# Optimization experiments

Measured on AMD Instinct MI355X. Metric: run time of the kernel, lower is better.

Reference implementation:

```python
import jax, jax.numpy as jnp
import numpy as np

B, L, ENC, EMB, H, V = 64, 33, 512, 256, 512, 32000


def setup_inputs() -> dict:
    key = jax.random.key(0)
    ks = jax.random.split(key, 16)
    x = jax.random.normal(ks[0], (B, ENC), dtype=jnp.float32)
    padded_target = jax.random.randint(ks[1], (B, L), 0, V)
    target_lengths = jax.random.randint(ks[2], (B,), 2, L + 1)
    target_lengths = target_lengths.at[0].set(L)  # pin max length -> static step count
    s = 0.05
    return {
        "x": x,
        "padded_target": padded_target,
        "target_lengths": target_lengths,
        "embed": jax.random.normal(ks[3], (V, EMB), dtype=jnp.float32) * s,
        "W_h0": jax.random.normal(ks[4], (H, ENC), dtype=jnp.float32) * s,
        "b_h0": jnp.zeros((H,), jnp.float32),
        "W_c0": jax.random.normal(ks[5], (H, ENC), dtype=jnp.float32) * s,
        "b_c0": jnp.zeros((H,), jnp.float32),
        "W_ih": jax.random.normal(ks[6], (4 * H, ENC + EMB), dtype=jnp.float32) * s,
        "W_hh": jax.random.normal(ks[7], (4 * H, H), dtype=jnp.float32) * s,
        "b_ih": jnp.zeros((4 * H,), jnp.float32),
        "b_hh": jnp.zeros((4 * H,), jnp.float32),
        "W_out": jax.random.normal(ks[8], (V, H), dtype=jnp.float32) * s,
        "b_out": jnp.zeros((V,), jnp.float32),
    }


def reference(x, padded_target, target_lengths, embed, W_h0, b_h0, W_c0, b_c0,
              W_ih, W_hh, b_ih, b_hh, W_out, b_out):
    # sort by length, descending (packed-sequence ordering)
    sorted_indices = jnp.argsort(-target_lengths)
    x = x[sorted_indices]                      # [B, ENC]
    tgt = padded_target[sorted_indices]        # [B, L]
    lens = target_lengths[sorted_indices] - 1  # decode steps per row
    emb = embed[tgt]                           # [B, L, EMB]

    h = x @ W_h0.T + b_h0                      # context-initialized state
    c = x @ W_c0.T + b_c0
    T = padded_target.shape[1] - 1             # static max steps (max len pinned to L)

    def step(carry, inp):
        h, c = carry
        e_t, t = inp
        active = (lens > t)[:, None]           # rows still decoding (prefix, sorted)
        g = jnp.concatenate([x, e_t], axis=1) @ W_ih.T + b_ih + h @ W_hh.T + b_hh
        i, f, gg, o = jnp.split(g, 4, axis=1)  # torch LSTMCell gate order i,f,g,o
        c_new = jax.nn.sigmoid(f) * c + jax.nn.sigmoid(i) * jnp.tanh(gg)
        h_new = jax.nn.sigmoid(o) * jnp.tanh(c_new)
        h = jnp.where(active, h_new, h)        # inactive rows keep frozen state
        c = jnp.where(active, c_new, c)
        pred = jnp.where(active, h_new @ W_out.T + b_out, 0.0)  # dropout p=0
        return (h, c), pred

    (_, _), preds = jax.lax.scan(
        step, (h, c), (jnp.transpose(emb[:, :T], (1, 0, 2)), jnp.arange(T)))
    prediction = jnp.transpose(preds, (1, 0, 2))  # [B, T, V]
    return prediction, sorted_indices
```

## Files before the change

kernel.cpp:

```cpp
#include <hip/hip_runtime.h>

typedef __attribute__((ext_vector_type(8))) short short8;
typedef __attribute__((ext_vector_type(8))) unsigned short ushort8;
typedef __attribute__((ext_vector_type(4))) float f32x4;
typedef __attribute__((ext_vector_type(4))) unsigned short ushort4v;

#define DEV __device__ __forceinline__

DEV unsigned short f2bf(float f) {
  unsigned int u = __float_as_uint(f);
  u += 0x7fffu + ((u >> 16) & 1u);
  return (unsigned short)(u >> 16);
}
DEV float sigm(float x) { return 1.f / (1.f + __expf(-x)); }
DEV float tanh_(float x) { return 1.f - 2.f / (1.f + __expf(2.f * x)); }

typedef __attribute__((address_space(1))) const void* as1cv;
typedef __attribute__((address_space(3))) void* as3v;
DEV void gll16(const void* g, void* l) {
  __builtin_amdgcn_global_load_lds((as1cv)g, (as3v)l, 16, 0, 0);
}

__global__ void __launch_bounds__(256) k_sort(const float* __restrict__ x,
    const int* __restrict__ ptar, const int* __restrict__ tlen,
    int* __restrict__ sidx, int* __restrict__ lens, int* __restrict__ tok,
    float* __restrict__ xs, float* __restrict__ tail) {
  __shared__ int ss[64];
  int tid = threadIdx.x;
  if (tid < 64) {
    int li = tlen[tid];
    int rank = 0;
    for (int j = 0; j < 64; ++j) {
      int lj = tlen[j];
      rank += (lj > li || (lj == li && j < tid)) ? 1 : 0;
    }
    ss[rank] = tid;
  }
  __syncthreads();
  if (tid < 64) {
    int src = ss[tid];
    sidx[tid] = src;
    lens[tid] = tlen[src] - 1;
    tail[tid] = (float)src;
  }
  __syncthreads();
  for (int idx = tid; idx < 32 * 64; idx += 256) {
    int t = idx >> 6, b = idx & 63;
    tok[idx] = ptar[ss[b] * 33 + t];
  }
  for (int idx = tid; idx < 64 * 512; idx += 256) {
    int b = idx >> 9;
    xs[idx] = x[ss[b] * 512 + (idx & 511)];
  }
}

__global__ void __launch_bounds__(256) k_convmany(
    const float* __restrict__ W_h0, const float* __restrict__ W_c0,
    const float* __restrict__ W_ih, const float* __restrict__ W_hh,
    const float* __restrict__ xs,
    unsigned short* __restrict__ Wpro, unsigned short* __restrict__ Wihb2,
    unsigned short* __restrict__ Whb, unsigned short* __restrict__ xsb) {
  long long g = (long long)(blockIdx.x * 256 + threadIdx.x) * 8;
  const float* src;
  unsigned short* dst;
  if (g < 262144) {
    src = W_h0 + g; dst = Wpro + g;
  } else if (g < 524288) {
    long long l = g - 262144; src = W_c0 + l; dst = Wpro + 262144 + l;
  } else if (g < 1572864) {
    long long l = g - 524288;
    long long r = l >> 9, c = l & 511;
    src = W_ih + r * 768 + c; dst = Wpro + 524288 + l;
  } else if (g < 2097152) {
    long long l = g - 1572864;
    long long r = l >> 8, c = l & 255;
    src = W_ih + r * 768 + 512 + c; dst = Wihb2 + l;
  } else if (g < 3145728) {
    long long l = g - 2097152; src = W_hh + l; dst = Whb + l;
  } else {
    long long l = g - 3145728; src = xs + l; dst = xsb + l;
  }
  float4 v0 = *(const float4*)src, v1 = *(const float4*)(src + 4);
  ushort8 o;
  o[0] = f2bf(v0.x); o[1] = f2bf(v0.y); o[2] = f2bf(v0.z); o[3] = f2bf(v0.w);
  o[4] = f2bf(v1.x); o[5] = f2bf(v1.y); o[6] = f2bf(v1.z); o[7] = f2bf(v1.w);
  *(ushort8*)dst = o;
}

__global__ void __launch_bounds__(256) k_conv(const float* __restrict__ W,
    unsigned short* __restrict__ Wb) {
  size_t i = (size_t)(blockIdx.x * 256 + threadIdx.x) * 4;
  float4 v = *(const float4*)(W + i);
  ushort4v o;
  o.x = f2bf(v.x); o.y = f2bf(v.y); o.z = f2bf(v.z); o.w = f2bf(v.w);
  *(ushort4v*)(Wb + i) = o;
}

__global__ void __launch_bounds__(256) k_pro(const unsigned short* __restrict__ xsb,
    const unsigned short* __restrict__ Wpro, const float* __restrict__ b_h0,
    const float* __restrict__ b_c0, const float* __restrict__ b_ih,
    const float* __restrict__ b_hh, unsigned short* __restrict__ h0b,
    float* __restrict__ c, float* __restrict__ gx) {
  int tid = threadIdx.x, lane = tid & 63, w = tid >> 6;
  int n0 = blockIdx.x * 64 + w * 16;
  int lr = lane & 15, lk = lane >> 4;
  f32x4 acc[4];
#pragma unroll
  for (int i = 0; i < 4; ++i) acc[i] = (f32x4){0.f, 0.f, 0.f, 0.f};
  const unsigned short* B = Wpro + (size_t)(n0 + lr) * 512 + lk * 8;
  const unsigned short* A = xsb + (size_t)lr * 512 + lk * 8;
#pragma unroll
  for (int ks = 0; ks < 16; ++ks) {
    short8 bfr = *(const short8*)(B + ks * 32);
#pragma unroll
    for (int mi = 0; mi < 4; ++mi) {
      short8 af = *(const short8*)(A + mi * 16 * 512 + ks * 32);
      acc[mi] = __builtin_amdgcn_mfma_f32_16x16x32_bf16(af, bfr, acc[mi], 0, 0, 0);
    }
  }
  int n = n0 + lr;
#pragma unroll
  for (int mi = 0; mi < 4; ++mi)
#pragma unroll
    for (int r = 0; r < 4; ++r) {
      int b = mi * 16 + lk * 4 + r;
      float v = acc[mi][r];
      if (n < 512) {
        h0b[b * 512 + n] = f2bf(v + b_h0[n]);
      } else if (n < 1024) {
        int u = n - 512;
        c[b * 512 + u] = v + b_c0[u];
      } else {
        int j = n - 1024;
        gx[(size_t)b * 2048 + j] = v + b_ih[j] + b_hh[j];
      }
    }
}

__global__ void __launch_bounds__(256) k_emb(const int* __restrict__ tok,
    const float* __restrict__ embed, unsigned short* __restrict__ Eb) {
  int gid = blockIdx.x * 256 + threadIdx.x;
  int row = gid >> 5, c8 = (gid & 31) * 8;
  const float* src = embed + (size_t)tok[row] * 256 + c8;
  float4 v0 = *(const float4*)src, v1 = *(const float4*)(src + 4);
  ushort8 o;
  o[0] = f2bf(v0.x); o[1] = f2bf(v0.y); o[2] = f2bf(v0.z); o[3] = f2bf(v0.w);
  o[4] = f2bf(v1.x); o[5] = f2bf(v1.y); o[6] = f2bf(v1.z); o[7] = f2bf(v1.w);
  *(ushort8*)(Eb + (size_t)row * 256 + c8) = o;
}

__global__ void __launch_bounds__(256) k_ga2(const unsigned short* __restrict__ Eb,
    const unsigned short* __restrict__ Wb2, const float* __restrict__ gx,
    float* __restrict__ GA) {
  __shared__ alignas(16) char ldsbuf[32768];
  char* ldsA = ldsbuf;
  char* ldsB = ldsbuf + 16384;
  int bid = blockIdx.x;
  int mt = bid & 15, nt = bid >> 4;
  int m0 = mt * 128, n0 = nt * 128;
  int tid = threadIdx.x, lane = tid & 63, w = tid >> 6;
  int wm = w >> 1, wn = w & 1;
  f32x4 acc[4][4];
#pragma unroll
  for (int a = 0; a < 4; ++a)
#pragma unroll
    for (int bq = 0; bq < 4; ++bq) acc[a][bq] = (f32x4){0.f, 0.f, 0.f, 0.f};
  const unsigned short* Arow = Eb + (size_t)m0 * 256;
  const unsigned short* Brow = Wb2 + (size_t)n0 * 256;
  for (int kt = 0; kt < 4; ++kt) {
    int k0 = kt * 64;
    if (kt) __syncthreads();
#pragma unroll
    for (int j = 0; j < 4; ++j) {
      int ci = j * 256 + w * 64 + lane;
      int r = ci >> 3;
      int clog = ((ci & 7) << 4) ^ ((r & 7) << 4);
      int ldst = (j * 256 + w * 64) * 16;
      gll16((const char*)(Arow + (size_t)r * 256 + k0) + clog, ldsA + ldst);
      gll16((const char*)(Brow + (size_t)r * 256 + k0) + clog, ldsB + ldst);
    }
    __syncthreads();
#pragma unroll
    for (int kk = 0; kk < 2; ++kk) {
      short8 af[4], bf[4];
      int cb = kk * 64 + (lane >> 4) * 16;
#pragma unroll
      for (int i = 0; i < 4; ++i) {
        int ar = wm * 64 + i * 16 + (lane & 15);
        af[i] = *(const short8*)(ldsA + ar * 128 + (cb ^ ((ar & 7) << 4)));
        int br = wn * 64 + i * 16 + (lane & 15);
        bf[i] = *(const short8*)(ldsB + br * 128 + (cb ^ ((br & 7) << 4)));
      }
#pragma unroll
      for (int mi = 0; mi < 4; ++mi)
#pragma unroll
        for (int ni = 0; ni < 4; ++ni)
          acc[mi][ni] = __builtin_amdgcn_mfma_f32_16x16x32_bf16(
              af[mi], bf[ni], acc[mi][ni], 0, 0, 0);
    }
  }
#pragma unroll
  for (int mi = 0; mi < 4; ++mi) {
    int mb = m0 + wm * 64 + mi * 16 + ((lane >> 4) << 2);
#pragma unroll
    for (int r = 0; r < 4; ++r) {
      int m = mb + r;
#pragma unroll
      for (int ni = 0; ni < 4; ++ni) {
        int j = n0 + wn * 64 + ni * 16 + (lane & 15);
        GA[(size_t)m * 2048 + j] = acc[mi][ni][r] + gx[(size_t)(m & 63) * 2048 + j];
      }
    }
  }
}

__global__ void __launch_bounds__(256) k_step2(
    const unsigned short* __restrict__ hin, unsigned short* __restrict__ hout,
    float* __restrict__ c, const float* __restrict__ GA,
    const unsigned short* __restrict__ Whb, const int* __restrict__ lens,
    unsigned short* __restrict__ Hm, int t) {
  __shared__ float Gs[4][32][16];
  int tid = threadIdx.x, lane = tid & 63, g = tid >> 6;
  int bk = blockIdx.x, mh = bk & 1, u0 = (bk >> 1) * 16;
  int lr = lane & 15, lk = lane >> 4;
  f32x4 acc[2];
  acc[0] = (f32x4){0.f, 0.f, 0.f, 0.f};
  acc[1] = (f32x4){0.f, 0.f, 0.f, 0.f};
  const unsigned short* B = Whb + (size_t)(g * 512 + u0 + lr) * 512 + lk * 8;
  const unsigned short* A = hin + (size_t)(mh * 32 + lr) * 512 + lk * 8;
#pragma unroll
  for (int ks = 0; ks < 16; ++ks) {
    short8 bfr = *(const short8*)(B + ks * 32);
    short8 a0 = *(const short8*)(A + ks * 32);
    short8 a1 = *(const short8*)(A + 16 * 512 + ks * 32);
    acc[0] = __builtin_amdgcn_mfma_f32_16x16x32_bf16(a0, bfr, acc[0], 0, 0, 0);
    acc[1] = __builtin_amdgcn_mfma_f32_16x16x32_bf16(a1, bfr, acc[1], 0, 0, 0);
  }
  const float* gab = GA + (size_t)(t * 64 + mh * 32) * 2048 + g * 512 + u0 + lr;
#pragma unroll
  for (int mi = 0; mi < 2; ++mi)
#pragma unroll
    for (int r = 0; r < 4; ++r) {
      int rl = mi * 16 + lk * 4 + r;
      Gs[g][rl][lr] = acc[mi][r] + gab[(size_t)rl * 2048];
    }
  __syncthreads();
#pragma unroll
  for (int cell = tid; cell < 512; cell += 256) {
    int row = cell >> 4, uc = cell & 15;
    int b = mh * 32 + row, u = u0 + uc;
    float fi = Gs[0][row][uc], ff = Gs[1][row][uc];
    float fg = Gs[2][row][uc], fo = Gs[3][row][uc];
    float cold = c[b * 512 + u];
    float cn = sigm(ff) * cold + sigm(fi) * tanh_(fg);
    float hn = sigm(fo) * tanh_(cn);
    bool act = lens[b] > t;
    if (act) c[b * 512 + u] = cn;
    unsigned short hb = f2bf(hn);
    hout[b * 512 + u] = act ? hb : hin[b * 512 + u];
    Hm[((size_t)b * 32 + t) * 512 + u] = act ? hb : (unsigned short)0;
  }
}

__global__ void __launch_bounds__(256) k_gemm(const unsigned short* __restrict__ Hm,
    const unsigned short* __restrict__ Wb, const float* __restrict__ b_out,
    const int* __restrict__ lens, float* __restrict__ out) {
  __shared__ alignas(16) char ldsbuf[32768];
  char* ldsA = ldsbuf;
  char* ldsB = ldsbuf + 16384;
  int bid = blockIdx.x;
  int mt = bid & 15, nt = bid >> 4;
  int m0 = mt * 128, n0 = nt * 128;
  int tid = threadIdx.x, lane = tid & 63, w = tid >> 6;
  int wm = w >> 1, wn = w & 1;
  f32x4 acc[4][4];
#pragma unroll
  for (int a = 0; a < 4; ++a)
#pragma unroll
    for (int bq = 0; bq < 4; ++bq) acc[a][bq] = (f32x4){0.f, 0.f, 0.f, 0.f};
  const unsigned short* Arow = Hm + (size_t)m0 * 512;
  const unsigned short* Brow = Wb + (size_t)n0 * 512;
  for (int kt = 0; kt < 8; ++kt) {
    int k0 = kt * 64;
    if (kt) __syncthreads();
#pragma unroll
    for (int j = 0; j < 4; ++j) {
      int ci = j * 256 + w * 64 + lane;
      int r = ci >> 3;
      int clog = ((ci & 7) << 4) ^ ((r & 7) << 4);
      int ldst = (j * 256 + w * 64) * 16;
      gll16((const char*)(Arow + (size_t)r * 512 + k0) + clog, ldsA + ldst);
      gll16((const char*)(Brow + (size_t)r * 512 + k0) + clog, ldsB + ldst);
    }
    __syncthreads();
#pragma unroll
    for (int kk = 0; kk < 2; ++kk) {
      short8 af[4], bf[4];
      int cb = kk * 64 + (lane >> 4) * 16;
#pragma unroll
      for (int i = 0; i < 4; ++i) {
        int ar = wm * 64 + i * 16 + (lane & 15);
        af[i] = *(const short8*)(ldsA + ar * 128 + (cb ^ ((ar & 7) << 4)));
        int br = wn * 64 + i * 16 + (lane & 15);
        bf[i] = *(const short8*)(ldsB + br * 128 + (cb ^ ((br & 7) << 4)));
      }
#pragma unroll
      for (int mi = 0; mi < 4; ++mi)
#pragma unroll
        for (int ni = 0; ni < 4; ++ni)
          acc[mi][ni] = __builtin_amdgcn_mfma_f32_16x16x32_bf16(
              af[mi], bf[ni], acc[mi][ni], 0, 0, 0);
    }
  }
#pragma unroll
  for (int mi = 0; mi < 4; ++mi) {
    int mb = m0 + wm * 64 + mi * 16 + ((lane >> 4) << 2);
#pragma unroll
    for (int r = 0; r < 4; ++r) {
      int m = mb + r;
      int b = m >> 5, t = m & 31;
      bool act = lens[b] > t;
      size_t orow = (size_t)m * 32000;
#pragma unroll
      for (int ni = 0; ni < 4; ++ni) {
        int n = n0 + wn * 64 + ni * 16 + (lane & 15);
        out[orow + n] = act ? (acc[mi][ni][r] + b_out[n]) : 0.f;
      }
    }
  }
}

extern "C" void kernel_launch(void* const* d_in, const int* in_sizes, int n_in,
                              void* d_out, int out_size, void* d_ws, size_t ws_size,
                              hipStream_t stream) {
  const float* x     = (const float*)d_in[0];
  const int*   ptar  = (const int*)d_in[1];
  const int*   tlen  = (const int*)d_in[2];
  const float* embed = (const float*)d_in[3];
  const float* W_h0  = (const float*)d_in[4];
  const float* b_h0  = (const float*)d_in[5];
  const float* W_c0  = (const float*)d_in[6];
  const float* b_c0  = (const float*)d_in[7];
  const float* W_ih  = (const float*)d_in[8];
  const float* W_hh  = (const float*)d_in[9];
  const float* b_ih  = (const float*)d_in[10];
  const float* b_hh  = (const float*)d_in[11];
  const float* W_out = (const float*)d_in[12];
  const float* b_out = (const float*)d_in[13];
  float* out = (float*)d_out;

  char* ws = (char*)d_ws;
  size_t off = 0;
  auto alloc = [&](size_t bytes) {
    void* p = ws + off;
    off += (bytes + 255) & ~(size_t)255;
    return p;
  };
  unsigned short* Wob = (unsigned short*)alloc(32000ull * 512 * 2);
  unsigned short* Hm  = (unsigned short*)alloc(2048ull * 512 * 2);
  float* xs   = (float*)alloc(64 * 512 * 4);
  unsigned short* h0b = (unsigned short*)alloc(64 * 512 * 2);
  unsigned short* h1b = (unsigned short*)alloc(64 * 512 * 2);
  float* cbuf = (float*)alloc(64 * 512 * 4);
  float* gx   = (float*)alloc(64 * 2048 * 4);
  int* sidx = (int*)alloc(64 * 4);
  int* lens = (int*)alloc(64 * 4);
  int* tok  = (int*)alloc(2048 * 4);

  float* GA = out;
  unsigned short* Wpro  = (unsigned short*)(out + 4194304);
  unsigned short* Wihb2 = (unsigned short*)(out + 4980736);
  unsigned short* Whb   = (unsigned short*)(out + 5242880);
  unsigned short* Eb    = (unsigned short*)(out + 5767168);
  unsigned short* xsb   = (unsigned short*)(out + 6029312);
  float* tail = out + 65536000;

  k_sort<<<1, 256, 0, stream>>>(x, ptar, tlen, sidx, lens, tok, xs, tail);
  k_convmany<<<1552, 256, 0, stream>>>(W_h0, W_c0, W_ih, W_hh, xs,
                                       Wpro, Wihb2, Whb, xsb);
  k_conv<<<16000, 256, 0, stream>>>(W_out, Wob);
  k_pro<<<48, 256, 0, stream>>>(xsb, Wpro, b_h0, b_c0, b_ih, b_hh, h0b, cbuf, gx);
  k_emb<<<256, 256, 0, stream>>>(tok, embed, Eb);
  k_ga2<<<256, 256, 0, stream>>>(Eb, Wihb2, gx, GA);

  unsigned short* hb[2] = {h0b, h1b};
  for (int t = 0; t < 32; ++t)
    k_step2<<<64, 256, 0, stream>>>(hb[t & 1], hb[(t + 1) & 1], cbuf, GA, Whb,
                                    lens, Hm, t);

  k_gemm<<<4000, 256, 0, stream>>>(Hm, Wob, b_out, lens, out);
  (void)in_sizes; (void)n_in; (void)out_size; (void)ws_size;
}
```

Before: 448.9 us.

## Compact active rows for output GEMM, fuse W_out conversion, retile step and GEMM

Builds a packed list of active (batch, step) rows so the vocabulary projection GEMM computes only the rows that are still decoding and scatters them back through an inverse index. Inactive output rows are zeroed by a separate fill kernel. The W_out bf16 conversion is merged into the gate-precompute kernel as extra blocks, and the recurrent step kernel is split into more blocks with smaller tiles. The GEMM moves to 512-thread blocks with 128x256 tiles and a grouped block order. This skips wasted GEMM work at the cost of scattered row writes and extra launches and indexing.

Result: faster. 362.4 us (-19.3%).

```diff
diff --git a/kernel.cpp b/kernel.cpp
--- a/kernel.cpp
+++ b/kernel.cpp
@@ -3,7 +3,6 @@
 typedef __attribute__((ext_vector_type(8))) short short8;
 typedef __attribute__((ext_vector_type(8))) unsigned short ushort8;
 typedef __attribute__((ext_vector_type(4))) float f32x4;
-typedef __attribute__((ext_vector_type(4))) unsigned short ushort4v;
 
 #define DEV __device__ __forceinline__
 
@@ -23,9 +22,10 @@
 
 __global__ void __launch_bounds__(256) k_sort(const float* __restrict__ x,
     const int* __restrict__ ptar, const int* __restrict__ tlen,
-    int* __restrict__ sidx, int* __restrict__ lens, int* __restrict__ tok,
+    int* __restrict__ sidx, int* __restrict__ lens, int* __restrict__ base,
+    int* __restrict__ inv, int* __restrict__ Pw, int* __restrict__ tok,
     float* __restrict__ xs, float* __restrict__ tail) {
-  __shared__ int ss[64];
+  __shared__ int ss[64], ls[64], bs[64];
   int tid = threadIdx.x;
   if (tid < 64) {
     int li = tlen[tid];
@@ -40,10 +40,22 @@
   if (tid < 64) {
     int src = ss[tid];
     sidx[tid] = src;
-    lens[tid] = tlen[src] - 1;
+    int l = tlen[src] - 1;
+    ls[tid] = l;
+    lens[tid] = l;
     tail[tid] = (float)src;
   }
   __syncthreads();
+  if (tid == 0) {
+    int s = 0;
+    for (int b = 0; b < 64; ++b) { bs[b] = s; base[b] = s; s += ls[b]; }
+    Pw[0] = s;
+  }
+  __syncthreads();
+  for (int idx = tid; idx < 2048; idx += 256) {
+    int b = idx >> 5, t = idx & 31;
+    if (t < ls[b]) inv[bs[b] + t] = idx;
+  }
   for (int idx = tid; idx < 32 * 64; idx += 256) {
     int t = idx >> 6, b = idx & 63;
     tok[idx] = ptar[ss[b] * 33 + t];
@@ -87,15 +99,6 @@
   *(ushort8*)dst = o;
 }
 
-__global__ void __launch_bounds__(256) k_conv(const float* __restrict__ W,
-    unsigned short* __restrict__ Wb) {
-  size_t i = (size_t)(blockIdx.x * 256 + threadIdx.x) * 4;
-  float4 v = *(const float4*)(W + i);
-  ushort4v o;
-  o.x = f2bf(v.x); o.y = f2bf(v.y); o.z = f2bf(v.z); o.w = f2bf(v.w);
-  *(ushort4v*)(Wb + i) = o;
-}
-
 __global__ void __launch_bounds__(256) k_pro(const unsigned short* __restrict__ xsb,
     const unsigned short* __restrict__ Wpro, const float* __restrict__ b_h0,
     const float* __restrict__ b_c0, const float* __restrict__ b_ih,
@@ -151,14 +154,30 @@
 
 __global__ void __launch_bounds__(256) k_ga2(const unsigned short* __restrict__ Eb,
     const unsigned short* __restrict__ Wb2, const float* __restrict__ gx,
-    float* __restrict__ GA) {
+    float* __restrict__ GA, const float* __restrict__ W_out,
+    unsigned short* __restrict__ Wob) {
+  int bid = blockIdx.x;
+  int tid = threadIdx.x;
+  if (bid >= 256) {
+    long long basei = (long long)(bid - 256) * 65536;
+#pragma unroll 4
+    for (int it = 0; it < 32; ++it) {
+      long long i = basei + (long long)it * 2048 + tid * 8;
+      float4 v0 = *(const float4*)(W_out + i);
+      float4 v1 = *(const float4*)(W_out + i + 4);
+      ushort8 o;
+      o[0] = f2bf(v0.x); o[1] = f2bf(v0.y); o[2] = f2bf(v0.z); o[3] = f2bf(v0.w);
+      o[4] = f2bf(v1.x); o[5] = f2bf(v1.y); o[6] = f2bf(v1.z); o[7] = f2bf(v1.w);
+      *(ushort8*)(Wob + i) = o;
+    }
+    return;
+  }
   __shared__ alignas(16) char ldsbuf[32768];
   char* ldsA = ldsbuf;
   char* ldsB = ldsbuf + 16384;
-  int bid = blockIdx.x;
   int mt = bid & 15, nt = bid >> 4;
   int m0 = mt * 128, n0 = nt * 128;
-  int tid = threadIdx.x, lane = tid & 63, w = tid >> 6;
+  int lane = tid & 63, w = tid >> 6;
   int wm = w >> 1, wn = w & 1;
   f32x4 acc[4][4];
 #pragma unroll
@@ -214,65 +233,74 @@
   }
 }
 
-__global__ void __launch_bounds__(256) k_step2(
+__global__ void __launch_bounds__(256) k_step3(
     const unsigned short* __restrict__ hin, unsigned short* __restrict__ hout,
     float* __restrict__ c, const float* __restrict__ GA,
     const unsigned short* __restrict__ Whb, const int* __restrict__ lens,
-    unsigned short* __restrict__ Hm, int t) {
-  __shared__ float Gs[4][32][16];
+    const int* __restrict__ base, unsigned short* __restrict__ Hm, int t) {
+  __shared__ float Gs[4][16][16];
   int tid = threadIdx.x, lane = tid & 63, g = tid >> 6;
-  int bk = blockIdx.x, mh = bk & 1, u0 = (bk >> 1) * 16;
   int lr = lane & 15, lk = lane >> 4;
-  f32x4 acc[2];
-  acc[0] = (f32x4){0.f, 0.f, 0.f, 0.f};
-  acc[1] = (f32x4){0.f, 0.f, 0.f, 0.f};
-  const unsigned short* B = Whb + (size_t)(g * 512 + u0 + lr) * 512 + lk * 8;
-  const unsigned short* A = hin + (size_t)(mh * 32 + lr) * 512 + lk * 8;
+  int mq = blockIdx.x & 3, ug = blockIdx.x >> 2;
+  int r0 = mq * 16, u0 = ug * 16;
+
+  const float* gab = GA + ((size_t)t * 64 + r0) * 2048 + g * 512 + u0 + lr;
+  float gv[4];
+#pragma unroll
+  for (int r = 0; r < 4; ++r) gv[r] = gab[(size_t)(lk * 4 + r) * 2048];
+
+  const unsigned short* Bp = Whb + (size_t)(g * 512 + u0 + lr) * 512 + lk * 8;
+  const unsigned short* Ap = hin + (size_t)(r0 + lr) * 512 + lk * 8;
+  f32x4 acc = (f32x4){0.f, 0.f, 0.f, 0.f};
 #pragma unroll
   for (int ks = 0; ks < 16; ++ks) {
-    short8 bfr = *(const short8*)(B + ks * 32);
-    short8 a0 = *(const short8*)(A + ks * 32);
-    short8 a1 = *(const short8*)(A + 16 * 512 + ks * 32);
-    acc[0] = __builtin_amdgcn_mfma_f32_16x16x32_bf16(a0, bfr, acc[0], 0, 0, 0);
-    acc[1] = __builtin_amdgcn_mfma_f32_16x16x32_bf16(a1, bfr, acc[1], 0, 0, 0);
-  }
-  const float* gab = GA + (size_t)(t * 64 + mh * 32) * 2048 + g * 512 + u0 + lr;
-#pragma unroll
-  for (int mi = 0; mi < 2; ++mi)
-#pragma unroll
-    for (int r = 0; r < 4; ++r) {
-      int rl = mi * 16 + lk * 4 + r;
-      Gs[g][rl][lr] = acc[mi][r] + gab[(size_t)rl * 2048];
-    }
+    short8 a0 = *(const short8*)(Ap + ks * 32);
+    short8 b0 = *(const short8*)(Bp + ks * 32);
+    acc = __builtin_amdgcn_mfma_f32_16x16x32_bf16(a0, b0, acc, 0, 0, 0);
+  }
+#pragma unroll
+  for (int r = 0; r < 4; ++r) Gs[g][lk * 4 + r][lr] = acc[r] + gv[r];
   __syncthreads();
-#pragma unroll
-  for (int cell = tid; cell < 512; cell += 256) {
-    int row = cell >> 4, uc = cell & 15;
-    int b = mh * 32 + row, u = u0 + uc;
-    float fi = Gs[0][row][uc], ff = Gs[1][row][uc];
-    float fg = Gs[2][row][uc], fo = Gs[3][row][uc];
-    float cold = c[b * 512 + u];
-    float cn = sigm(ff) * cold + sigm(fi) * tanh_(fg);
-    float hn = sigm(fo) * tanh_(cn);
-    bool act = lens[b] > t;
-    if (act) c[b * 512 + u] = cn;
-    unsigned short hb = f2bf(hn);
-    hout[b * 512 + u] = act ? hb : hin[b * 512 + u];
-    Hm[((size_t)b * 32 + t) * 512 + u] = act ? hb : (unsigned short)0;
-  }
-}
-
-__global__ void __launch_bounds__(256) k_gemm(const unsigned short* __restrict__ Hm,
+
+  int row = tid >> 4, uc = tid & 15;
+  int b = r0 + row, u = u0 + uc;
+  float fi = Gs[0][row][uc], ff = Gs[1][row][uc];
+  float fg = Gs[2][row][uc], fo = Gs[3][row][uc];
+  float cold = c[b * 512 + u];
+  float cn = sigm(ff) * cold + sigm(fi) * tanh_(fg);
+  float hn = sigm(fo) * tanh_(cn);
+  bool act = lens[b] > t;
+  if (act) c[b * 512 + u] = cn;
+  unsigned short hbv = f2bf(hn);
+  hout[b * 512 + u] = act ? hbv : hin[b * 512 + u];
+  if (act) Hm[((size_t)(base[b] + t)) * 512 + u] = hbv;
+}
+
+__global__ void __launch_bounds__(256) k_zf(const int* __restrict__ lens,
+    float* __restrict__ out) {
+  int m = blockIdx.x;
+  int b = m >> 5, t = m & 31;
+  if (lens[b] > t) return;
+  float4 z = {0.f, 0.f, 0.f, 0.f};
+  float* row = out + (size_t)m * 32000;
+  for (int i = threadIdx.x * 4; i < 32000; i += 1024)
+    *(float4*)(row + i) = z;
+}
+
+__global__ void __launch_bounds__(512) k_gemm(const unsigned short* __restrict__ Hm,
     const unsigned short* __restrict__ Wb, const float* __restrict__ b_out,
-    const int* __restrict__ lens, float* __restrict__ out) {
-  __shared__ alignas(16) char ldsbuf[32768];
+    const int* __restrict__ inv, const int* __restrict__ Pw,
+    float* __restrict__ out) {
+  __shared__ alignas(16) char ldsbuf[49152];
   char* ldsA = ldsbuf;
   char* ldsB = ldsbuf + 16384;
-  int bid = blockIdx.x;
-  int mt = bid & 15, nt = bid >> 4;
-  int m0 = mt * 128, n0 = nt * 128;
+  int P = Pw[0];
+  int sb = (blockIdx.x & 7) * 250 + (blockIdx.x >> 3);
+  int mt = sb % 16, nt = sb / 16;
+  int m0 = mt * 128, n0 = nt * 256;
+  if (m0 >= P) return;
   int tid = threadIdx.x, lane = tid & 63, w = tid >> 6;
-  int wm = w >> 1, wn = w & 1;
+  int wm = w >> 2, wn = w & 3;
   f32x4 acc[4][4];
 #pragma unroll
   for (int a = 0; a < 4; ++a)
@@ -284,13 +312,18 @@
     int k0 = kt * 64;
     if (kt) __syncthreads();
 #pragma unroll
-    for (int j = 0; j < 4; ++j) {
-      int ci = j * 256 + w * 64 + lane;
+    for (int j = 0; j < 2; ++j) {
+      int ci = j * 512 + tid;
       int r = ci >> 3;
       int clog = ((ci & 7) << 4) ^ ((r & 7) << 4);
-      int ldst = (j * 256 + w * 64) * 16;
-      gll16((const char*)(Arow + (size_t)r * 512 + k0) + clog, ldsA + ldst);
-      gll16((const char*)(Brow + (size_t)r * 512 + k0) + clog, ldsB + ldst);
+      gll16((const char*)(Arow + (size_t)r * 512 + k0) + clog, ldsA + ci * 16);
+    }
+#pragma unroll
+    for (int j = 0; j < 4; ++j) {
+      int ci = j * 512 + tid;
+      int r = ci >> 3;
+      int clog = ((ci & 7) << 4) ^ ((r & 7) << 4);
+      gll16((const char*)(Brow + (size_t)r * 512 + k0) + clog, ldsB + ci * 16);
     }
     __syncthreads();
 #pragma unroll
@@ -314,17 +347,16 @@
   }
 #pragma unroll
   for (int mi = 0; mi < 4; ++mi) {
-    int mb = m0 + wm * 64 + mi * 16 + ((lane >> 4) << 2);
+    int pb = m0 + wm * 64 + mi * 16 + ((lane >> 4) << 2);
 #pragma unroll
     for (int r = 0; r < 4; ++r) {
-      int m = mb + r;
-      int b = m >> 5, t = m & 31;
-      bool act = lens[b] > t;
-      size_t orow = (size_t)m * 32000;
+      int p = pb + r;
+      if (p >= P) continue;
+      size_t orow = (size_t)inv[p] * 32000;
 #pragma unroll
       for (int ni = 0; ni < 4; ++ni) {
         int n = n0 + wn * 64 + ni * 16 + (lane & 15);
-        out[orow + n] = act ? (acc[mi][ni][r] + b_out[n]) : 0.f;
+        out[orow + n] = acc[mi][ni][r] + b_out[n];
       }
     }
   }
@@ -365,6 +397,9 @@
   float* gx   = (float*)alloc(64 * 2048 * 4);
   int* sidx = (int*)alloc(64 * 4);
   int* lens = (int*)alloc(64 * 4);
+  int* base = (int*)alloc(64 * 4);
+  int* inv  = (int*)alloc(2048 * 4);
+  int* Pw   = (int*)alloc(4);
   int* tok  = (int*)alloc(2048 * 4);
 
   float* GA = out;
@@ -375,19 +410,20 @@
   unsigned short* xsb   = (unsigned short*)(out + 6029312);
   float* tail = out + 65536000;
 
-  k_sort<<<1, 256, 0, stream>>>(x, ptar, tlen, sidx, lens, tok, xs, tail);
+  k_sort<<<1, 256, 0, stream>>>(x, ptar, tlen, sidx, lens, base, inv, Pw, tok,
+                                xs, tail);
   k_convmany<<<1552, 256, 0, stream>>>(W_h0, W_c0, W_ih, W_hh, xs,
                                        Wpro, Wihb2, Whb, xsb);
-  k_conv<<<16000, 256, 0, stream>>>(W_out, Wob);
   k_pro<<<48, 256, 0, stream>>>(xsb, Wpro, b_h0, b_c0, b_ih, b_hh, h0b, cbuf, gx);
   k_emb<<<256, 256, 0, stream>>>(tok, embed, Eb);
-  k_ga2<<<256, 256, 0, stream>>>(Eb, Wihb2, gx, GA);
+  k_ga2<<<506, 256, 0, stream>>>(Eb, Wihb2, gx, GA, W_out, Wob);
 
   unsigned short* hb[2] = {h0b, h1b};
   for (int t = 0; t < 32; ++t)
-    k_step2<<<64, 256, 0, stream>>>(hb[t & 1], hb[(t + 1) & 1], cbuf, GA, Whb,
-                                    lens, Hm, t);
-
-  k_gemm<<<4000, 256, 0, stream>>>(Hm, Wob, b_out, lens, out);
+    k_step3<<<128, 256, 0, stream>>>(hb[t & 1], hb[(t + 1) & 1], cbuf, GA, Whb,
+                                     lens, base, Hm, t);
+
+  k_zf<<<2048, 256, 0, stream>>>(lens, out);
+  k_gemm<<<2000, 512, 0, stream>>>(Hm, Wob, b_out, inv, Pw, out);
   (void)in_sizes; (void)n_in; (void)out_size; (void)ws_size;
 }
```
